# Kernel optimization log

Measured on AMD Instinct MI355X. Metric: run time of the kernel, lower is better.

Reference implementation:

```python
import jax, jax.numpy as jnp
import numpy as np
import math

HIDDEN = 4096
N_HEADS = 32
N_KV_HEADS = 8
HEAD_DIM = HIDDEN // N_HEADS  # 128
N_GROUPS = N_HEADS // N_KV_HEADS  # 4
ROPE_THETA = 10000.0


def setup_inputs() -> dict:
    key = jax.random.key(0)
    ks = jax.random.split(key, 5)
    B, S = 2, 2048
    hidden_states = jax.random.normal(ks[0], (B, S, HIDDEN), dtype=jnp.float32)
    position_ids = jnp.broadcast_to(jnp.arange(S, dtype=jnp.int32)[None, :], (B, S))
    sc = 1.0 / math.sqrt(HIDDEN)
    Wq = jax.random.normal(ks[1], (HIDDEN, N_HEADS * HEAD_DIM), dtype=jnp.float32) * sc
    Wk = jax.random.normal(ks[2], (HIDDEN, N_KV_HEADS * HEAD_DIM), dtype=jnp.float32) * sc
    Wv = jax.random.normal(ks[3], (HIDDEN, N_KV_HEADS * HEAD_DIM), dtype=jnp.float32) * sc
    Wo = jax.random.normal(ks[4], (HIDDEN, HIDDEN), dtype=jnp.float32) * sc
    return {"hidden_states": hidden_states, "position_ids": position_ids,
            "Wq": Wq, "Wk": Wk, "Wv": Wv, "Wo": Wo}


def _rope_cos_sin(position_ids):
    # inv_freq: [head_dim//2]
    inv_freq = 1.0 / (ROPE_THETA ** (jnp.arange(0, HEAD_DIM, 2, dtype=jnp.float32) / HEAD_DIM))
    freqs = position_ids.astype(jnp.float32)[..., None] * inv_freq  # [B, S, hd/2]
    emb = jnp.concatenate([freqs, freqs], axis=-1)  # [B, S, hd]
    return jnp.cos(emb), jnp.sin(emb)


def _rotate_half(x):
    h = x.shape[-1] // 2
    return jnp.concatenate([-x[..., h:], x[..., :h]], axis=-1)


def _apply_rope(x, cos, sin):
    # x: [B, H, S, hd]; cos/sin: [B, S, hd] -> unsqueeze head dim
    return x * cos[:, None] + _rotate_half(x) * sin[:, None]


def reference(hidden_states, position_ids, Wq, Wk, Wv, Wo):
    B, S, _ = hidden_states.shape
    q = (hidden_states @ Wq).reshape(B, S, N_HEADS, HEAD_DIM).transpose(0, 2, 1, 3)
    k = (hidden_states @ Wk).reshape(B, S, N_KV_HEADS, HEAD_DIM).transpose(0, 2, 1, 3)
    v = (hidden_states @ Wv).reshape(B, S, N_KV_HEADS, HEAD_DIM).transpose(0, 2, 1, 3)

    cos, sin = _rope_cos_sin(position_ids)
    q = _apply_rope(q, cos, sin)
    k = _apply_rope(k, cos, sin)

    # repeat_kv: (B, kvH, S, d) -> (B, H, S, d)
    k = jnp.repeat(k, N_GROUPS, axis=1)
    v = jnp.repeat(v, N_GROUPS, axis=1)

    scores = jnp.einsum('bhqd,bhkd->bhqk', q, k) / math.sqrt(HEAD_DIM)
    causal = jnp.tril(jnp.ones((S, S), dtype=bool))
    neg = jnp.finfo(jnp.float32).min
    scores = jnp.where(causal[None, None], scores, neg)
    attn = jax.nn.softmax(scores.astype(jnp.float32), axis=-1).astype(q.dtype)

    out = jnp.einsum('bhqk,bhkd->bhqd', attn, v)
    out = out.transpose(0, 2, 1, 3).reshape(B, S, HIDDEN)
    return out @ Wo
```

## Files before the change

kernel.cpp:

```cpp
#include <hip/hip_runtime.h>
#include <hip/hip_bf16.h>
#include <math.h>

#define HIDDEN 4096
#define NH 32
#define NKV 8
#define HD 128
#define S_LEN 2048
#define BATCH 2
#define MROWS (BATCH * S_LEN)
#define QKVW 6144

typedef __attribute__((ext_vector_type(8))) __bf16 bf16x8;
typedef __attribute__((ext_vector_type(4))) float f32x4;

__device__ __forceinline__ f32x4 mfma16(bf16x8 a, bf16x8 b, f32x4 c) {
  return __builtin_amdgcn_mfma_f32_16x16x32_bf16(a, b, c, 0, 0, 0);
}

__device__ __forceinline__ void gload16(const __bf16* g, const __bf16* l) {
  __builtin_amdgcn_global_load_lds(
      (const __attribute__((address_space(1))) void*)g,
      (__attribute__((address_space(3))) void*)l, 16, 0, 0);
}

#define SBAR()                              \
  do {                                      \
    asm volatile("" ::: "memory");          \
    __builtin_amdgcn_s_barrier();           \
    asm volatile("" ::: "memory");          \
  } while (0)

#define VMCNT8() asm volatile("s_waitcnt vmcnt(8)" ::: "memory")
#define VMCNT6() asm volatile("s_waitcnt vmcnt(6)" ::: "memory")

__global__ __launch_bounds__(256) void cvt_kernel(const float* __restrict__ in,
                                                  __bf16* __restrict__ out, int n) {
  int i = (blockIdx.x * 256 + threadIdx.x) * 8;
  if (i >= n) return;
  float4 a = *reinterpret_cast<const float4*>(in + i);
  float4 b = *reinterpret_cast<const float4*>(in + i + 4);
  bf16x8 t;
  t[0] = (__bf16)a.x; t[1] = (__bf16)a.y; t[2] = (__bf16)a.z; t[3] = (__bf16)a.w;
  t[4] = (__bf16)b.x; t[5] = (__bf16)b.y; t[6] = (__bf16)b.z; t[7] = (__bf16)b.w;
  *reinterpret_cast<bf16x8*>(out + i) = t;
}

__global__ __launch_bounds__(256) void tcvt3_kernel(const float* __restrict__ Wq,
                                                    const float* __restrict__ Wk,
                                                    const float* __restrict__ Wv,
                                                    __bf16* __restrict__ Wt) {
  __shared__ float t[32][33];
  int z = blockIdx.z;
  const float* in;
  __bf16* out;
  int C;
  if (z == 0)      { in = Wq; out = Wt;                         C = 4096; }
  else if (z == 1) { in = Wk; out = Wt + (size_t)4096 * 4096;   C = 1024; }
  else             { in = Wv; out = Wt + (size_t)5120 * 4096;   C = 1024; }
  if ((int)blockIdx.x * 32 >= C) return;
  int tx = threadIdx.x, ty = threadIdx.y;
  int r0 = blockIdx.y * 32, c0 = blockIdx.x * 32;
#pragma unroll
  for (int i = 0; i < 4; i++)
    t[ty + i * 8][tx] = in[(size_t)(r0 + ty + i * 8) * C + c0 + tx];
  __syncthreads();
#pragma unroll
  for (int i = 0; i < 4; i++)
    out[(size_t)(c0 + ty + i * 8) * 4096 + r0 + tx] = (__bf16)t[tx][ty + i * 8];
}

__global__ __launch_bounds__(256) void tcvt_f32(const float* __restrict__ in,
                                                __bf16* __restrict__ out,
                                                int R, int C) {
  __shared__ float t[32][33];
  int tx = threadIdx.x, ty = threadIdx.y;
  int r0 = blockIdx.y * 32, c0 = blockIdx.x * 32;
#pragma unroll
  for (int i = 0; i < 4; i++)
    t[ty + i * 8][tx] = in[(size_t)(r0 + ty + i * 8) * C + c0 + tx];
  __syncthreads();
#pragma unroll
  for (int i = 0; i < 4; i++)
    out[(size_t)(c0 + ty + i * 8) * R + r0 + tx] = (__bf16)t[tx][ty + i * 8];
}

__global__ __launch_bounds__(256) void tvt_kernel(const __bf16* __restrict__ qkv,
                                                  __bf16* __restrict__ vt) {
  __shared__ __bf16 t[32][33];
  int tx = threadIdx.x, ty = threadIdx.y;
  int z = blockIdx.z;
  int b = z >> 3, kvh = z & 7;
  int kv0 = blockIdx.y * 32, d0 = blockIdx.x * 32;
#pragma unroll
  for (int i = 0; i < 4; i++)
    t[ty + i * 8][tx] =
        qkv[(size_t)(b * S_LEN + kv0 + ty + i * 8) * QKVW + 5120 + kvh * HD + d0 + tx];
  __syncthreads();
  int cperm = kv0 + 2 * (tx & 15) + (tx >> 4);
#pragma unroll
  for (int i = 0; i < 4; i++)
    vt[((size_t)z * HD + d0 + ty + i * 8) * S_LEN + cperm] = t[tx][ty + i * 8];
}

template<typename CT>
__global__ __launch_bounds__(512, 2) void gemm256(const __bf16* __restrict__ A,
                                                  const __bf16* __restrict__ Bt,
                                                  CT* __restrict__ C,
                                                  int K, int ldc, int nbx) {
  __shared__ char lds[131072];
  const int tid = threadIdx.x;
  const int l = tid & 63, w = tid >> 6;
  const int lrow = l & 15, lg = l >> 4;
  const int sw = (lrow & 7) << 4;

  int nwg = gridDim.x;
  int swz = (blockIdx.x & 7) * (nwg >> 3) + (blockIdx.x >> 3);
  int bx = swz % nbx, by = swz / nbx;
  int m0 = by * 256, n0 = bx * 256;

  const int rA = w * 8 + (l >> 3);
  const int csw = ((l & 7) ^ (l >> 3)) * 8;
  const __bf16* As_[2][2];
  const __bf16* Bs_[2][2];
#pragma unroll
  for (int h = 0; h < 2; h++)
#pragma unroll
    for (int p = 0; p < 2; p++) {
      As_[h][p] = A + (size_t)(m0 + h * 128 + p * 64 + rA) * K + csw;
      Bs_[h][p] = Bt + (size_t)(n0 + h * 128 + p * 64 + rA) * K + csw;
    }

  auto stageA = [&](int par, int h, int kt) {
#pragma unroll
    for (int p = 0; p < 2; p++)
      gload16(As_[h][p] + kt * 64,
              (const __bf16*)(lds + par * 32768 + h * 16384 + p * 8192 + w * 1024));
  };
  auto stageB = [&](int par, int h, int kt) {
#pragma unroll
    for (int p = 0; p < 2; p++)
      gload16(Bs_[h][p] + kt * 64,
              (const __bf16*)(lds + 65536 + par * 32768 + h * 16384 + p * 8192 + w * 1024));
  };

  const int arbase = (w >> 2) * 64 + lrow;
  const int brbase = (w & 3) * 32 + lrow;

  bf16x8 aA[4][2];
  bf16x8 bB[2][2][2];

  auto readA = [&](int par, int ah) {
#pragma unroll
    for (int i = 0; i < 4; i++)
#pragma unroll
      for (int kk = 0; kk < 2; kk++)
        aA[i][kk] = *reinterpret_cast<const bf16x8*>(
            lds + par * 32768 + (arbase + i * 16 + ah * 128) * 128 +
            ((kk * 64 + lg * 16) ^ sw));
  };
  auto readB = [&](int par, int bh) {
#pragma unroll
    for (int j = 0; j < 2; j++)
#pragma unroll
      for (int kk = 0; kk < 2; kk++)
        bB[bh][j][kk] = *reinterpret_cast<const bf16x8*>(
            lds + 65536 + par * 32768 + (brbase + j * 16 + bh * 128) * 128 +
            ((kk * 64 + lg * 16) ^ sw));
  };

  f32x4 acc[8][4];
#pragma unroll
  for (int i = 0; i < 8; i++)
#pragma unroll
    for (int j = 0; j < 4; j++) {
      acc[i][j][0] = 0.f; acc[i][j][1] = 0.f; acc[i][j][2] = 0.f; acc[i][j][3] = 0.f;
    }

  const int NT = K >> 6;

  stageA(0, 0, 0); stageB(0, 0, 0);
  stageA(0, 1, 0); stageB(0, 1, 0);
  stageA(1, 0, 1); stageB(1, 0, 1);
  VMCNT8();
  SBAR();

#define MFMA_QUAD(AH, BH)                                                   \
  __builtin_amdgcn_s_setprio(1);                                            \
  _Pragma("unroll") for (int i4 = 0; i4 < 4; i4++)                          \
      _Pragma("unroll") for (int j2 = 0; j2 < 2; j2++)                      \
          _Pragma("unroll") for (int kk = 0; kk < 2; kk++)                  \
              acc[(AH)*4 + i4][(BH)*2 + j2] =                               \
                  mfma16(aA[i4][kk], bB[BH][j2][kk], acc[(AH)*4 + i4][(BH)*2 + j2]); \
  __builtin_amdgcn_s_setprio(0);

#define GTILE256(PAR, TT)                                                   \
  {                                                                         \
    const int t1n = ((TT) + 1 < NT) ? (TT) + 1 : 0;                         \
    const int t2n = ((TT) + 2 < NT) ? (TT) + 2 : 0;                         \
    readA(PAR, 0);                                                          \
    readB(PAR, 0);                                                          \
    stageA(PAR ^ 1, 1, t1n);                                                \
    stageB(PAR ^ 1, 1, t1n);                                                \
    VMCNT8();                                                               \
    SBAR();                                                                 \
    MFMA_QUAD(0, 0);                                                        \
    SBAR();                                                                 \
    readB(PAR, 1);                                                          \
    stageA(PAR, 0, t2n);                                                    \
    SBAR();                                                                 \
    MFMA_QUAD(0, 1);                                                        \
    SBAR();                                                                 \
    readA(PAR, 1);                                                          \
    stageB(PAR, 0, t2n);                                                    \
    SBAR();                                                                 \
    MFMA_QUAD(1, 0);                                                        \
    MFMA_QUAD(1, 1);                                                        \
    VMCNT8();                                                               \
    SBAR();                                                                 \
  }

  for (int t = 0; t < NT; t += 2) {
    GTILE256(0, t);
    GTILE256(1, t + 1);
  }
#undef GTILE256
#undef MFMA_QUAD

#pragma unroll
  for (int i = 0; i < 8; i++) {
    int row = m0 + (w >> 2) * 64 + (i & 3) * 16 + (i >> 2) * 128 + lg * 4;
#pragma unroll
    for (int j = 0; j < 4; j++) {
      int col = n0 + (w & 3) * 32 + (j & 1) * 16 + (j >> 1) * 128 + lrow;
#pragma unroll
      for (int jj = 0; jj < 4; jj++)
        C[(size_t)(row + jj) * ldc + col] = (CT)acc[i][j][jj];
    }
  }
}

template<typename CT>
__global__ __launch_bounds__(512, 2) void gemm128(const __bf16* __restrict__ A,
                                                  const __bf16* __restrict__ Bt,
                                                  CT* __restrict__ C,
                                                  int K, int ldc, int nbx) {
  __shared__ char lds[98304];
  const int tid = threadIdx.x;
  const int l = tid & 63, w = tid >> 6;
  const int lrow = l & 15, lg = l >> 4;
  const int sw = (lrow & 7) << 4;

  int nwg = gridDim.x;
  int swz = (blockIdx.x & 7) * (nwg >> 3) + (blockIdx.x >> 3);
  int bx = swz % nbx, by = swz / nbx;
  int m0 = by * 256, n0 = bx * 128;

  const int rA = w * 8 + (l >> 3);
  const int csw = ((l & 7) ^ (l >> 3)) * 8;
  const __bf16* As_[2][2];
  const __bf16* Bs_[2];
#pragma unroll
  for (int h = 0; h < 2; h++)
#pragma unroll
    for (int p = 0; p < 2; p++)
      As_[h][p] = A + (size_t)(m0 + h * 128 + p * 64 + rA) * K + csw;
#pragma unroll
  for (int p = 0; p < 2; p++)
    Bs_[p] = Bt + (size_t)(n0 + p * 64 + rA) * K + csw;

  auto stageA = [&](int par, int h, int kt) {
#pragma unroll
    for (int p = 0; p < 2; p++)
      gload16(As_[h][p] + kt * 64,
              (const __bf16*)(lds + par * 32768 + h * 16384 + p * 8192 + w * 1024));
  };
  auto stageB = [&](int par, int kt) {
#pragma unroll
    for (int p = 0; p < 2; p++)
      gload16(Bs_[p] + kt * 64,
              (const __bf16*)(lds + 65536 + par * 16384 + p * 8192 + w * 1024));
  };

  const int arbase = (w >> 2) * 64 + lrow;
  const int brbase = (w & 3) * 32 + lrow;

  bf16x8 aA[4][2];
  bf16x8 bB[2][2];

  auto readA = [&](int par, int ah) {
#pragma unroll
    for (int i = 0; i < 4; i++)
#pragma unroll
      for (int kk = 0; kk < 2; kk++)
        aA[i][kk] = *reinterpret_cast<const bf16x8*>(
            lds + par * 32768 + (arbase + i * 16 + ah * 128) * 128 +
            ((kk * 64 + lg * 16) ^ sw));
  };
  auto readB = [&](int par) {
#pragma unroll
    for (int j = 0; j < 2; j++)
#pragma unroll
      for (int kk = 0; kk < 2; kk++)
        bB[j][kk] = *reinterpret_cast<const bf16x8*>(
            lds + 65536 + par * 16384 + (brbase + j * 16) * 128 +
            ((kk * 64 + lg * 16) ^ sw));
  };

  f32x4 acc[8][2];
#pragma unroll
  for (int i = 0; i < 8; i++)
#pragma unroll
    for (int j = 0; j < 2; j++) {
      acc[i][j][0] = 0.f; acc[i][j][1] = 0.f; acc[i][j][2] = 0.f; acc[i][j][3] = 0.f;
    }

  const int NT = K >> 6;

  stageA(0, 0, 0); stageB(0, 0);
  stageA(0, 1, 0); stageB(1, 1); stageA(1, 0, 1);
  VMCNT6();
  SBAR();

#define MFMA_HALF(AH)                                                        \
  __builtin_amdgcn_s_setprio(1);                                             \
  _Pragma("unroll") for (int i4 = 0; i4 < 4; i4++)                           \
      _Pragma("unroll") for (int j2 = 0; j2 < 2; j2++)                       \
          _Pragma("unroll") for (int kk = 0; kk < 2; kk++)                   \
              acc[(AH)*4 + i4][j2] =                                         \
                  mfma16(aA[i4][kk], bB[j2][kk], acc[(AH)*4 + i4][j2]);      \
  __builtin_amdgcn_s_setprio(0);

#define GTILE128(PAR, TT)                                                    \
  {                                                                          \
    const int t1n = ((TT) + 1 < NT) ? (TT) + 1 : 0;                          \
    const int t2n = ((TT) + 2 < NT) ? (TT) + 2 : 0;                          \
    readA(PAR, 0);                                                           \
    readB(PAR);                                                              \
    stageA(PAR ^ 1, 1, t1n);                                                 \
    VMCNT6();                                                                \
    SBAR();                                                                  \
    MFMA_HALF(0);                                                            \
    SBAR();                                                                  \
    readA(PAR, 1);                                                           \
    stageB(PAR, t2n);                                                        \
    stageA(PAR, 0, t2n);                                                     \
    SBAR();                                                                  \
    MFMA_HALF(1);                                                            \
    VMCNT6();                                                                \
    SBAR();                                                                  \
  }

  for (int t = 0; t < NT; t += 2) {
    GTILE128(0, t);
    GTILE128(1, t + 1);
  }
#undef GTILE128
#undef MFMA_HALF

#pragma unroll
  for (int i = 0; i < 8; i++) {
    int row = m0 + (w >> 2) * 64 + (i & 3) * 16 + (i >> 2) * 128 + lg * 4;
#pragma unroll
    for (int j = 0; j < 2; j++) {
      int col = n0 + (w & 3) * 32 + j * 16 + lrow;
#pragma unroll
      for (int jj = 0; jj < 4; jj++)
        C[(size_t)(row + jj) * ldc + col] = (CT)acc[i][j][jj];
    }
  }
}

__global__ __launch_bounds__(256) void ropek_kernel(__bf16* __restrict__ qkv,
                                                    const int* __restrict__ pos) {
  int row = blockIdx.x * 4 + (threadIdx.x >> 6);
  int t = threadIdx.x & 63;
  float p = (float)pos[row];
  int head = t >> 3, chunk = t & 7;
  __bf16* base = qkv + (size_t)row * QKVW + 4096 + head * HD + chunk * 8;
  bf16x8 x1 = *reinterpret_cast<const bf16x8*>(base);
  bf16x8 x2 = *reinterpret_cast<const bf16x8*>(base + 64);
  bf16x8 o1, o2;
#pragma unroll
  for (int e = 0; e < 8; e++) {
    float ang = p * exp2f(-0.20762050f * (float)(chunk * 8 + e));
    float s, c;
    __sincosf(ang, &s, &c);
    float a = (float)x1[e], b2 = (float)x2[e];
    o1[e] = (__bf16)(a * c - b2 * s);
    o2[e] = (__bf16)(b2 * c + a * s);
  }
  *reinterpret_cast<bf16x8*>(base) = o1;
  *reinterpret_cast<bf16x8*>(base + 64) = o2;
}

__global__ __launch_bounds__(512) void attn_kernel(const __bf16* __restrict__ qkv,
                                                   const __bf16* __restrict__ vt,
                                                   const int* __restrict__ pos,
                                                   __bf16* __restrict__ out) {
  __shared__ __bf16 Ks[64 * 128];
  __shared__ __bf16 Vs[128 * 64];

  int tid = threadIdx.x;
  int l = tid & 63, w = tid >> 6;
  int bid = blockIdx.x;
  int qblk = 7 - (bid >> 6);
  int rem = bid & 63;
  int h = rem & 31, b = rem >> 5;
  int kvh = h >> 2;
  int q0w = qblk * 256 + w * 32;
  int lrow = l & 15, lg = l >> 4;
  int sw = (lrow & 7) << 4;
  const float SCL = 0.08838834764831845f * 1.4426950408889634f;

  const __bf16* kbase = qkv + (size_t)(b * S_LEN) * QKVW + 4096 + kvh * HD;
  const __bf16* vbase = vt + ((size_t)(b * NKV + kvh) * HD) * S_LEN;

  int krow = tid >> 3;
  int kslot = (tid & 7) * 2;
  int vrow = tid >> 2;
  int vslot = (tid & 3) * 2;
  char* KsB = (char*)Ks;
  char* VsB = (char*)Vs;
  int koff0 = krow * 256 + ((kslot * 16) ^ ((krow & 7) << 4));
  int koff1 = krow * 256 + (((kslot + 1) * 16) ^ ((krow & 7) << 4));
  int voff0 = vrow * 128 + ((vslot * 16) ^ ((vrow & 7) << 4));
  int voff1 = vrow * 128 + (((vslot + 1) * 16) ^ ((vrow & 7) << 4));
  const __bf16* kg = kbase + (size_t)krow * QKVW + kslot * 8;
  const __bf16* vg = vbase + (size_t)vrow * S_LEN + vslot * 8;

  bf16x8 qf[2][4];
#pragma unroll
  for (int mi = 0; mi < 2; mi++) {
    int qrow = q0w + mi * 16 + lrow;
    const __bf16* qp = qkv + (size_t)(b * S_LEN + qrow) * QKVW + h * HD + lg * 8;
    float p = (float)pos[b * S_LEN + qrow];
#pragma unroll
    for (int kk = 0; kk < 2; kk++) {
      bf16x8 xlo = *reinterpret_cast<const bf16x8*>(qp + kk * 32);
      bf16x8 xhi = *reinterpret_cast<const bf16x8*>(qp + (kk + 2) * 32);
      bf16x8 olo, ohi;
#pragma unroll
      for (int e = 0; e < 8; e++) {
        int d = kk * 32 + lg * 8 + e;
        float ang = p * exp2f(-0.20762050f * (float)d);
        float s, c;
        __sincosf(ang, &s, &c);
        c *= SCL; s *= SCL;
        float a = (float)xlo[e], b2 = (float)xhi[e];
        olo[e] = (__bf16)(a * c - b2 * s);
        ohi[e] = (__bf16)(b2 * c + a * s);
      }
      qf[mi][kk] = olo;
      qf[mi][kk + 2] = ohi;
    }
  }

  f32x4 ov[2][8];
#pragma unroll
  for (int mi = 0; mi < 2; mi++)
#pragma unroll
    for (int n = 0; n < 8; n++) {
      ov[mi][n][0] = 0.f; ov[mi][n][1] = 0.f; ov[mi][n][2] = 0.f; ov[mi][n][3] = 0.f;
    }
  float m[2], ssum[2];
  m[0] = -3.0e38f; m[1] = -3.0e38f;
  ssum[0] = 0.f; ssum[1] = 0.f;

  int nt = 4 * qblk + 4;
  bf16x8 kr0, kr1, vr0, vr1;

  kr0 = *reinterpret_cast<const bf16x8*>(kg);
  kr1 = *reinterpret_cast<const bf16x8*>(kg + 8);
  vr0 = *reinterpret_cast<const bf16x8*>(vg);
  vr1 = *reinterpret_cast<const bf16x8*>(vg + 8);
  *reinterpret_cast<bf16x8*>(KsB + koff0) = kr0;
  *reinterpret_cast<bf16x8*>(KsB + koff1) = kr1;
  *reinterpret_cast<bf16x8*>(VsB + voff0) = vr0;
  *reinterpret_cast<bf16x8*>(VsB + voff1) = vr1;
  __syncthreads();

  for (int t = 0;; t++) {
    int kv0 = t * 64;
    bool more = (t + 1 < nt);
    if (more) {
      int kvn = kv0 + 64;
      kr0 = *reinterpret_cast<const bf16x8*>(kg + (size_t)kvn * QKVW);
      kr1 = *reinterpret_cast<const bf16x8*>(kg + (size_t)kvn * QKVW + 8);
      vr0 = *reinterpret_cast<const bf16x8*>(vg + kvn);
      vr1 = *reinterpret_cast<const bf16x8*>(vg + kvn + 8);
    }

    bool active = (kv0 <= q0w + 31);
    if (active) {
      f32x4 sc[2][4];
#pragma unroll
      for (int mi = 0; mi < 2; mi++)
#pragma unroll
        for (int c = 0; c < 4; c++) {
          sc[mi][c][0] = 0.f; sc[mi][c][1] = 0.f; sc[mi][c][2] = 0.f; sc[mi][c][3] = 0.f;
        }
#pragma unroll
      for (int c = 0; c < 4; c++) {
        int rb = (c * 16 + lrow) * 256;
#pragma unroll
        for (int kk = 0; kk < 4; kk++) {
          bf16x8 kf = *reinterpret_cast<const bf16x8*>(KsB + rb + ((kk * 64 + lg * 16) ^ sw));
          sc[0][c] = mfma16(kf, qf[0][kk], sc[0][c]);
          sc[1][c] = mfma16(kf, qf[1][kk], sc[1][c]);
        }
      }

      bool bound = (kv0 + 64 > q0w);
      if (bound) {
#pragma unroll
        for (int mi = 0; mi < 2; mi++) {
          int qidx = q0w + mi * 16 + lrow;
#pragma unroll
          for (int jj = 0; jj < 4; jj++) {
            int kvb = kv0 + lg * 4 + jj;
            if (kvb > qidx)      sc[mi][0][jj] = -3.0e38f;
            if (kvb + 16 > qidx) sc[mi][1][jj] = -3.0e38f;
            if (kvb + 32 > qidx) sc[mi][2][jj] = -3.0e38f;
            if (kvb + 48 > qidx) sc[mi][3][jj] = -3.0e38f;
          }
        }
      }

      float lm[2];
      bool lanegrow = false;
#pragma unroll
      for (int mi = 0; mi < 2; mi++) {
        float a0 = fmaxf(fmaxf(sc[mi][0][0], sc[mi][0][1]), fmaxf(sc[mi][0][2], sc[mi][0][3]));
        float a1 = fmaxf(fmaxf(sc[mi][1][0], sc[mi][1][1]), fmaxf(sc[mi][1][2], sc[mi][1][3]));
        float a2 = fmaxf(fmaxf(sc[mi][2][0], sc[mi][2][1]), fmaxf(sc[mi][2][2], sc[mi][2][3]));
        float a3 = fmaxf(fmaxf(sc[mi][3][0], sc[mi][3][1]), fmaxf(sc[mi][3][2], sc[mi][3][3]));
        lm[mi] = fmaxf(fmaxf(a0, a1), fmaxf(a2, a3));
        lanegrow |= (lm[mi] > m[mi] + 8.0f);
      }

      if (__any(lanegrow)) {
        float es[2];
#pragma unroll
        for (int mi = 0; mi < 2; mi++) {
          float r = lm[mi];
          r = fmaxf(r, __shfl_xor(r, 16));
          r = fmaxf(r, __shfl_xor(r, 32));
          float mo = m[mi];
          bool grow = (r > mo + 8.0f);
          float mn = grow ? r : mo;
          float e = grow ? exp2f(mo - r) : 1.0f;
          es[mi] = e;
          m[mi] = mn;
          ssum[mi] *= e;
        }
        float esv[2][4];
#pragma unroll
        for (int mi = 0; mi < 2; mi++)
#pragma unroll
          for (int jj = 0; jj < 4; jj++)
            esv[mi][jj] = __shfl(es[mi], lg * 4 + jj);
#pragma unroll
        for (int mi = 0; mi < 2; mi++)
#pragma unroll
          for (int n = 0; n < 8; n++)
#pragma unroll
            for (int jj = 0; jj < 4; jj++) ov[mi][n][jj] *= esv[mi][jj];
      }

      bf16x8 pa[2][2];
#pragma unroll
      for (int mi = 0; mi < 2; mi++) {
        float mn = m[mi];
#pragma unroll
        for (int c = 0; c < 4; c++)
#pragma unroll
          for (int r = 0; r < 4; r++) {
            float p = exp2f(sc[mi][c][r] - mn);
            ssum[mi] += p;
            pa[mi][c >> 1][(r << 1) | (c & 1)] = (__bf16)p;
          }
      }

#pragma unroll
      for (int kvs = 0; kvs < 2; kvs++) {
#pragma unroll
        for (int n = 0; n < 8; n++) {
          bf16x8 vf = *reinterpret_cast<const bf16x8*>(
              VsB + (n * 16 + lrow) * 128 + ((kvs * 64 + lg * 16) ^ sw));
          ov[0][n] = mfma16(pa[0][kvs], vf, ov[0][n]);
          ov[1][n] = mfma16(pa[1][kvs], vf, ov[1][n]);
        }
      }
    }

    if (!more) break;
    __syncthreads();
    *reinterpret_cast<bf16x8*>(KsB + koff0) = kr0;
    *reinterpret_cast<bf16x8*>(KsB + koff1) = kr1;
    *reinterpret_cast<bf16x8*>(VsB + voff0) = vr0;
    *reinterpret_cast<bf16x8*>(VsB + voff1) = vr1;
    __syncthreads();
  }

  float rs[2];
#pragma unroll
  for (int mi = 0; mi < 2; mi++) {
    float s = ssum[mi];
    s += __shfl_xor(s, 16);
    s += __shfl_xor(s, 32);
    rs[mi] = s;
  }
  float rinv[2][4];
#pragma unroll
  for (int mi = 0; mi < 2; mi++)
#pragma unroll
    for (int jj = 0; jj < 4; jj++)
      rinv[mi][jj] = 1.0f / __shfl(rs[mi], lg * 4 + jj);
#pragma unroll
  for (int mi = 0; mi < 2; mi++)
#pragma unroll
    for (int n = 0; n < 8; n++)
#pragma unroll
      for (int jj = 0; jj < 4; jj++) {
        out[(size_t)(b * S_LEN + q0w + mi * 16 + lg * 4 + jj) * HIDDEN + h * HD + n * 16 + lrow] =
            (__bf16)(ov[mi][n][jj] * rinv[mi][jj]);
      }
}

extern "C" void kernel_launch(void* const* d_in, const int* in_sizes, int n_in,
                              void* d_out, int out_size, void* d_ws, size_t ws_size,
                              hipStream_t stream) {
  const float* hidden = (const float*)d_in[0];
  const int* posids   = (const int*)d_in[1];
  const float* Wq     = (const float*)d_in[2];
  const float* Wk     = (const float*)d_in[3];
  const float* Wv     = (const float*)d_in[4];
  const float* Wo     = (const float*)d_in[5];
  float* out = (float*)d_out;

  char* ws = (char*)d_ws;
  __bf16* h_bf    = (__bf16*)(ws + 0);
  __bf16* a_buf   = h_bf;
  __bf16* Wt      = (__bf16*)(ws + 33554432);
  __bf16* qkv_buf = (__bf16*)(ws + 83886080);
  __bf16* vt_buf  = (__bf16*)(ws + 134217728);

  dim3 b256(256), b328(32, 8), b512(512);

  cvt_kernel<<<dim3(MROWS * HIDDEN / (256 * 8)), b256, 0, stream>>>(hidden, h_bf, MROWS * HIDDEN);

  tcvt3_kernel<<<dim3(128, 128, 3), b328, 0, stream>>>(Wq, Wk, Wv, Wt);

  gemm256<__bf16><<<dim3(256), b512, 0, stream>>>(
      h_bf, Wt, qkv_buf, HIDDEN, QKVW, 4096 / 256);
  gemm128<__bf16><<<dim3(256), b512, 0, stream>>>(
      h_bf, Wt + (size_t)4096 * 4096, qkv_buf + 4096, HIDDEN, QKVW, 2048 / 128);

  ropek_kernel<<<dim3(MROWS / 4), b256, 0, stream>>>(qkv_buf, posids);

  tvt_kernel<<<dim3(HD / 32, S_LEN / 32, BATCH * NKV), b328, 0, stream>>>(qkv_buf, vt_buf);

  attn_kernel<<<dim3(8 * NH * BATCH), b512, 0, stream>>>(qkv_buf, vt_buf, posids, a_buf);

  tcvt_f32<<<dim3(HIDDEN / 32, HIDDEN / 32), b328, 0, stream>>>(Wo, Wt, HIDDEN, HIDDEN);

  gemm256<float><<<dim3(256), b512, 0, stream>>>(
      a_buf, Wt, out, HIDDEN, HIDDEN, HIDDEN / 256);
}
```

Baseline: 451.2 us.

## Double-buffer attention K/V tiles in LDS via direct global-to-LDS loads

Replaces the register-staged K/V prefetch (global load to registers, then LDS store between two barriers) with global_load_lds directly into a double-buffered 64KB LDS region. The swizzle moves to the global address side so the LDS layout matches the existing read pattern. Each iteration now needs one vmcnt(0) wait and one barrier instead of two barriers plus LDS stores, and registers are freed. The cost is twice the LDS footprint, which may limit blocks per CU.

```diff
diff --git a/kernel.cpp b/kernel.cpp
--- a/kernel.cpp
+++ b/kernel.cpp
@@ -33,6 +33,7 @@
 
 #define VMCNT8() asm volatile("s_waitcnt vmcnt(8)" ::: "memory")
 #define VMCNT6() asm volatile("s_waitcnt vmcnt(6)" ::: "memory")
+#define VMCNT0() asm volatile("s_waitcnt vmcnt(0)" ::: "memory")
 
 __global__ __launch_bounds__(256) void cvt_kernel(const float* __restrict__ in,
                                                   __bf16* __restrict__ out, int n) {
@@ -398,8 +399,7 @@
                                                    const __bf16* __restrict__ vt,
                                                    const int* __restrict__ pos,
                                                    __bf16* __restrict__ out) {
-  __shared__ __bf16 Ks[64 * 128];
-  __shared__ __bf16 Vs[128 * 64];
+  __shared__ char lds[65536];
 
   int tid = threadIdx.x;
   int l = tid & 63, w = tid >> 6;
@@ -416,18 +416,24 @@
   const __bf16* kbase = qkv + (size_t)(b * S_LEN) * QKVW + 4096 + kvh * HD;
   const __bf16* vbase = vt + ((size_t)(b * NKV + kvh) * HD) * S_LEN;
 
-  int krow = tid >> 3;
-  int kslot = (tid & 7) * 2;
-  int vrow = tid >> 2;
-  int vslot = (tid & 3) * 2;
-  char* KsB = (char*)Ks;
-  char* VsB = (char*)Vs;
-  int koff0 = krow * 256 + ((kslot * 16) ^ ((krow & 7) << 4));
-  int koff1 = krow * 256 + (((kslot + 1) * 16) ^ ((krow & 7) << 4));
-  int voff0 = vrow * 128 + ((vslot * 16) ^ ((vrow & 7) << 4));
-  int voff1 = vrow * 128 + (((vslot + 1) * 16) ^ ((vrow & 7) << 4));
-  const __bf16* kg = kbase + (size_t)krow * QKVW + kslot * 8;
-  const __bf16* vg = vbase + (size_t)vrow * S_LEN + vslot * 8;
+  int rK0 = 8 * w + (l >> 4), rK1 = rK0 + 4;
+  int cK0 = (l & 8) | (((l & 7) ^ (rK0 & 7)) & 7);
+  int cK1 = (l & 8) | (((l & 7) ^ (rK1 & 7)) & 7);
+  const __bf16* kgs0 = kbase + (size_t)rK0 * QKVW + cK0 * 8;
+  const __bf16* kgs1 = kbase + (size_t)rK1 * QKVW + cK1 * 8;
+  int rV0 = 16 * w + (l >> 3), rV1 = rV0 + 8;
+  int cV0 = (l & 7) ^ (rV0 & 7);
+  int cV1 = (l & 7) ^ (rV1 & 7);
+  const __bf16* vgs0 = vbase + (size_t)rV0 * S_LEN + cV0 * 8;
+  const __bf16* vgs1 = vbase + (size_t)rV1 * S_LEN + cV1 * 8;
+
+  auto stageKV = [&](int par, int kvn) {
+    size_t ko = (size_t)kvn * QKVW;
+    gload16(kgs0 + ko, (const __bf16*)(lds + par * 16384 + w * 2048));
+    gload16(kgs1 + ko, (const __bf16*)(lds + par * 16384 + w * 2048 + 1024));
+    gload16(vgs0 + kvn, (const __bf16*)(lds + 32768 + par * 16384 + w * 2048));
+    gload16(vgs1 + kvn, (const __bf16*)(lds + 32768 + par * 16384 + w * 2048 + 1024));
+  };
 
   bf16x8 qf[2][4];
 #pragma unroll
@@ -468,28 +474,16 @@
   ssum[0] = 0.f; ssum[1] = 0.f;
 
   int nt = 4 * qblk + 4;
-  bf16x8 kr0, kr1, vr0, vr1;
-
-  kr0 = *reinterpret_cast<const bf16x8*>(kg);
-  kr1 = *reinterpret_cast<const bf16x8*>(kg + 8);
-  vr0 = *reinterpret_cast<const bf16x8*>(vg);
-  vr1 = *reinterpret_cast<const bf16x8*>(vg + 8);
-  *reinterpret_cast<bf16x8*>(KsB + koff0) = kr0;
-  *reinterpret_cast<bf16x8*>(KsB + koff1) = kr1;
-  *reinterpret_cast<bf16x8*>(VsB + voff0) = vr0;
-  *reinterpret_cast<bf16x8*>(VsB + voff1) = vr1;
+
+  stageKV(0, 0);
+  VMCNT0();
   __syncthreads();
 
   for (int t = 0;; t++) {
     int kv0 = t * 64;
     bool more = (t + 1 < nt);
-    if (more) {
-      int kvn = kv0 + 64;
-      kr0 = *reinterpret_cast<const bf16x8*>(kg + (size_t)kvn * QKVW);
-      kr1 = *reinterpret_cast<const bf16x8*>(kg + (size_t)kvn * QKVW + 8);
-      vr0 = *reinterpret_cast<const bf16x8*>(vg + kvn);
-      vr1 = *reinterpret_cast<const bf16x8*>(vg + kvn + 8);
-    }
+    if (more) stageKV((t + 1) & 1, kv0 + 64);
+    int pb = (t & 1) * 16384;
 
     bool active = (kv0 <= q0w + 31);
     if (active) {
@@ -502,10 +496,10 @@
         }
 #pragma unroll
       for (int c = 0; c < 4; c++) {
-        int rb = (c * 16 + lrow) * 256;
+        int rb = pb + (c * 16 + lrow) * 256;
 #pragma unroll
         for (int kk = 0; kk < 4; kk++) {
-          bf16x8 kf = *reinterpret_cast<const bf16x8*>(KsB + rb + ((kk * 64 + lg * 16) ^ sw));
+          bf16x8 kf = *reinterpret_cast<const bf16x8*>(lds + rb + ((kk * 64 + lg * 16) ^ sw));
           sc[0][c] = mfma16(kf, qf[0][kk], sc[0][c]);
           sc[1][c] = mfma16(kf, qf[1][kk], sc[1][c]);
         }
@@ -587,7 +581,7 @@
 #pragma unroll
         for (int n = 0; n < 8; n++) {
           bf16x8 vf = *reinterpret_cast<const bf16x8*>(
-              VsB + (n * 16 + lrow) * 128 + ((kvs * 64 + lg * 16) ^ sw));
+              lds + 32768 + pb + (n * 16 + lrow) * 128 + ((kvs * 64 + lg * 16) ^ sw));
           ov[0][n] = mfma16(pa[0][kvs], vf, ov[0][n]);
           ov[1][n] = mfma16(pa[1][kvs], vf, ov[1][n]);
         }
@@ -595,11 +589,7 @@
     }
 
     if (!more) break;
-    __syncthreads();
-    *reinterpret_cast<bf16x8*>(KsB + koff0) = kr0;
-    *reinterpret_cast<bf16x8*>(KsB + koff1) = kr1;
-    *reinterpret_cast<bf16x8*>(VsB + voff0) = vr0;
-    *reinterpret_cast<bf16x8*>(VsB + voff1) = vr1;
+    VMCNT0();
     __syncthreads();
   }
 
```

After: 452.5 us. Within noise of the previous version (+0.3%).

## Halve attention query tile to 128 rows per block, 16 per wave

Applied to the files above, without the earlier changes.

The attention kernel now gives each block 128 query rows instead of 256, with each wave handling one 16-row MFMA tile instead of two. The grid doubles to 1024 blocks, which should improve load balance across CUs for the causal triangle and lower per-thread register use. In exchange, each K/V tile loaded into LDS is reused by half as many query rows, so K/V traffic doubles and there is less MFMA work per LDS read.

```diff
diff --git a/kernel.cpp b/kernel.cpp
--- a/kernel.cpp
+++ b/kernel.cpp
@@ -404,11 +404,11 @@
   int tid = threadIdx.x;
   int l = tid & 63, w = tid >> 6;
   int bid = blockIdx.x;
-  int qblk = 7 - (bid >> 6);
+  int qblk = 15 - (bid >> 6);
   int rem = bid & 63;
   int h = rem & 31, b = rem >> 5;
   int kvh = h >> 2;
-  int q0w = qblk * 256 + w * 32;
+  int q0w = qblk * 128 + w * 16;
   int lrow = l & 15, lg = l >> 4;
   int sw = (lrow & 7) << 4;
   const float SCL = 0.08838834764831845f * 1.4426950408889634f;
@@ -429,10 +429,9 @@
   const __bf16* kg = kbase + (size_t)krow * QKVW + kslot * 8;
   const __bf16* vg = vbase + (size_t)vrow * S_LEN + vslot * 8;
 
-  bf16x8 qf[2][4];
-#pragma unroll
-  for (int mi = 0; mi < 2; mi++) {
-    int qrow = q0w + mi * 16 + lrow;
+  bf16x8 qf[4];
+  {
+    int qrow = q0w + lrow;
     const __bf16* qp = qkv + (size_t)(b * S_LEN + qrow) * QKVW + h * HD + lg * 8;
     float p = (float)pos[b * S_LEN + qrow];
 #pragma unroll
@@ -451,23 +450,19 @@
         olo[e] = (__bf16)(a * c - b2 * s);
         ohi[e] = (__bf16)(b2 * c + a * s);
       }
-      qf[mi][kk] = olo;
-      qf[mi][kk + 2] = ohi;
-    }
-  }
-
-  f32x4 ov[2][8];
-#pragma unroll
-  for (int mi = 0; mi < 2; mi++)
-#pragma unroll
-    for (int n = 0; n < 8; n++) {
-      ov[mi][n][0] = 0.f; ov[mi][n][1] = 0.f; ov[mi][n][2] = 0.f; ov[mi][n][3] = 0.f;
-    }
-  float m[2], ssum[2];
-  m[0] = -3.0e38f; m[1] = -3.0e38f;
-  ssum[0] = 0.f; ssum[1] = 0.f;
-
-  int nt = 4 * qblk + 4;
+      qf[kk] = olo;
+      qf[kk + 2] = ohi;
+    }
+  }
+
+  f32x4 ov[8];
+#pragma unroll
+  for (int n = 0; n < 8; n++) {
+    ov[n][0] = 0.f; ov[n][1] = 0.f; ov[n][2] = 0.f; ov[n][3] = 0.f;
+  }
+  float m = -3.0e38f, ssum = 0.f;
+
+  int nt = 2 * qblk + 2;
   bf16x8 kr0, kr1, vr0, vr1;
 
   kr0 = *reinterpret_cast<const bf16x8*>(kg);
@@ -491,96 +486,72 @@
       vr1 = *reinterpret_cast<const bf16x8*>(vg + kvn + 8);
     }
 
-    bool active = (kv0 <= q0w + 31);
+    bool active = (kv0 <= q0w + 15);
     if (active) {
-      f32x4 sc[2][4];
-#pragma unroll
-      for (int mi = 0; mi < 2; mi++)
-#pragma unroll
-        for (int c = 0; c < 4; c++) {
-          sc[mi][c][0] = 0.f; sc[mi][c][1] = 0.f; sc[mi][c][2] = 0.f; sc[mi][c][3] = 0.f;
-        }
+      f32x4 sc[4];
+#pragma unroll
+      for (int c = 0; c < 4; c++) {
+        sc[c][0] = 0.f; sc[c][1] = 0.f; sc[c][2] = 0.f; sc[c][3] = 0.f;
+      }
 #pragma unroll
       for (int c = 0; c < 4; c++) {
         int rb = (c * 16 + lrow) * 256;
 #pragma unroll
         for (int kk = 0; kk < 4; kk++) {
           bf16x8 kf = *reinterpret_cast<const bf16x8*>(KsB + rb + ((kk * 64 + lg * 16) ^ sw));
-          sc[0][c] = mfma16(kf, qf[0][kk], sc[0][c]);
-          sc[1][c] = mfma16(kf, qf[1][kk], sc[1][c]);
+          sc[c] = mfma16(kf, qf[kk], sc[c]);
         }
       }
 
       bool bound = (kv0 + 64 > q0w);
       if (bound) {
-#pragma unroll
-        for (int mi = 0; mi < 2; mi++) {
-          int qidx = q0w + mi * 16 + lrow;
-#pragma unroll
-          for (int jj = 0; jj < 4; jj++) {
-            int kvb = kv0 + lg * 4 + jj;
-            if (kvb > qidx)      sc[mi][0][jj] = -3.0e38f;
-            if (kvb + 16 > qidx) sc[mi][1][jj] = -3.0e38f;
-            if (kvb + 32 > qidx) sc[mi][2][jj] = -3.0e38f;
-            if (kvb + 48 > qidx) sc[mi][3][jj] = -3.0e38f;
-          }
+        int qidx = q0w + lrow;
+#pragma unroll
+        for (int jj = 0; jj < 4; jj++) {
+          int kvb = kv0 + lg * 4 + jj;
+          if (kvb > qidx)      sc[0][jj] = -3.0e38f;
+          if (kvb + 16 > qidx) sc[1][jj] = -3.0e38f;
+          if (kvb + 32 > qidx) sc[2][jj] = -3.0e38f;
+          if (kvb + 48 > qidx) sc[3][jj] = -3.0e38f;
         }
       }
 
-      float lm[2];
-      bool lanegrow = false;
-#pragma unroll
-      for (int mi = 0; mi < 2; mi++) {
-        float a0 = fmaxf(fmaxf(sc[mi][0][0], sc[mi][0][1]), fmaxf(sc[mi][0][2], sc[mi][0][3]));
-        float a1 = fmaxf(fmaxf(sc[mi][1][0], sc[mi][1][1]), fmaxf(sc[mi][1][2], sc[mi][1][3]));
-        float a2 = fmaxf(fmaxf(sc[mi][2][0], sc[mi][2][1]), fmaxf(sc[mi][2][2], sc[mi][2][3]));
-        float a3 = fmaxf(fmaxf(sc[mi][3][0], sc[mi][3][1]), fmaxf(sc[mi][3][2], sc[mi][3][3]));
-        lm[mi] = fmaxf(fmaxf(a0, a1), fmaxf(a2, a3));
-        lanegrow |= (lm[mi] > m[mi] + 8.0f);
+      float a0 = fmaxf(fmaxf(sc[0][0], sc[0][1]), fmaxf(sc[0][2], sc[0][3]));
+      float a1 = fmaxf(fmaxf(sc[1][0], sc[1][1]), fmaxf(sc[1][2], sc[1][3]));
+      float a2 = fmaxf(fmaxf(sc[2][0], sc[2][1]), fmaxf(sc[2][2], sc[2][3]));
+      float a3 = fmaxf(fmaxf(sc[3][0], sc[3][1]), fmaxf(sc[3][2], sc[3][3]));
+      float lm = fmaxf(fmaxf(a0, a1), fmaxf(a2, a3));
+      bool lanegrow = (lm > m + 8.0f);
+
+      if (__any(lanegrow)) {
+        float r = lm;
+        r = fmaxf(r, __shfl_xor(r, 16));
+        r = fmaxf(r, __shfl_xor(r, 32));
+        float mo = m;
+        bool grow = (r > mo + 8.0f);
+        float mn = grow ? r : mo;
+        float e = grow ? exp2f(mo - r) : 1.0f;
+        m = mn;
+        ssum *= e;
+        float esv[4];
+#pragma unroll
+        for (int jj = 0; jj < 4; jj++)
+          esv[jj] = __shfl(e, lg * 4 + jj);
+#pragma unroll
+        for (int n = 0; n < 8; n++)
+#pragma unroll
+          for (int jj = 0; jj < 4; jj++) ov[n][jj] *= esv[jj];
       }
 
-      if (__any(lanegrow)) {
-        float es[2];
-#pragma unroll
-        for (int mi = 0; mi < 2; mi++) {
-          float r = lm[mi];
-          r = fmaxf(r, __shfl_xor(r, 16));
-          r = fmaxf(r, __shfl_xor(r, 32));
-          float mo = m[mi];
-          bool grow = (r > mo + 8.0f);
-          float mn = grow ? r : mo;
-          float e = grow ? exp2f(mo - r) : 1.0f;
-          es[mi] = e;
-          m[mi] = mn;
-          ssum[mi] *= e;
+      bf16x8 pa[2];
+#pragma unroll
+      for (int c = 0; c < 4; c++)
+#pragma unroll
+        for (int r = 0; r < 4; r++) {
+          float p = exp2f(sc[c][r] - m);
+          ssum += p;
+          pa[c >> 1][(r << 1) | (c & 1)] = (__bf16)p;
         }
-        float esv[2][4];
-#pragma unroll
-        for (int mi = 0; mi < 2; mi++)
-#pragma unroll
-          for (int jj = 0; jj < 4; jj++)
-            esv[mi][jj] = __shfl(es[mi], lg * 4 + jj);
-#pragma unroll
-        for (int mi = 0; mi < 2; mi++)
-#pragma unroll
-          for (int n = 0; n < 8; n++)
-#pragma unroll
-            for (int jj = 0; jj < 4; jj++) ov[mi][n][jj] *= esv[mi][jj];
-      }
-
-      bf16x8 pa[2][2];
-#pragma unroll
-      for (int mi = 0; mi < 2; mi++) {
-        float mn = m[mi];
-#pragma unroll
-        for (int c = 0; c < 4; c++)
-#pragma unroll
-          for (int r = 0; r < 4; r++) {
-            float p = exp2f(sc[mi][c][r] - mn);
-            ssum[mi] += p;
-            pa[mi][c >> 1][(r << 1) | (c & 1)] = (__bf16)p;
-          }
-      }
 
 #pragma unroll
       for (int kvs = 0; kvs < 2; kvs++) {
@@ -588,8 +559,7 @@
         for (int n = 0; n < 8; n++) {
           bf16x8 vf = *reinterpret_cast<const bf16x8*>(
               VsB + (n * 16 + lrow) * 128 + ((kvs * 64 + lg * 16) ^ sw));
-          ov[0][n] = mfma16(pa[0][kvs], vf, ov[0][n]);
-          ov[1][n] = mfma16(pa[1][kvs], vf, ov[1][n]);
+          ov[n] = mfma16(pa[kvs], vf, ov[n]);
         }
       }
     }
@@ -603,29 +573,20 @@
     __syncthreads();
   }
 
-  float rs[2];
-#pragma unroll
-  for (int mi = 0; mi < 2; mi++) {
-    float s = ssum[mi];
-    s += __shfl_xor(s, 16);
-    s += __shfl_xor(s, 32);
-    rs[mi] = s;
-  }
-  float rinv[2][4];
-#pragma unroll
-  for (int mi = 0; mi < 2; mi++)
-#pragma unroll
-    for (int jj = 0; jj < 4; jj++)
-      rinv[mi][jj] = 1.0f / __shfl(rs[mi], lg * 4 + jj);
-#pragma unroll
-  for (int mi = 0; mi < 2; mi++)
-#pragma unroll
-    for (int n = 0; n < 8; n++)
-#pragma unroll
-      for (int jj = 0; jj < 4; jj++) {
-        out[(size_t)(b * S_LEN + q0w + mi * 16 + lg * 4 + jj) * HIDDEN + h * HD + n * 16 + lrow] =
-            (__bf16)(ov[mi][n][jj] * rinv[mi][jj]);
-      }
+  float s = ssum;
+  s += __shfl_xor(s, 16);
+  s += __shfl_xor(s, 32);
+  float rinv[4];
+#pragma unroll
+  for (int jj = 0; jj < 4; jj++)
+    rinv[jj] = 1.0f / __shfl(s, lg * 4 + jj);
+#pragma unroll
+  for (int n = 0; n < 8; n++)
+#pragma unroll
+    for (int jj = 0; jj < 4; jj++) {
+      out[(size_t)(b * S_LEN + q0w + lg * 4 + jj) * HIDDEN + h * HD + n * 16 + lrow] =
+          (__bf16)(ov[n][jj] * rinv[jj]);
+    }
 }
 
 extern "C" void kernel_launch(void* const* d_in, const int* in_sizes, int n_in,
@@ -661,7 +622,7 @@
 
   tvt_kernel<<<dim3(HD / 32, S_LEN / 32, BATCH * NKV), b328, 0, stream>>>(qkv_buf, vt_buf);
 
-  attn_kernel<<<dim3(8 * NH * BATCH), b512, 0, stream>>>(qkv_buf, vt_buf, posids, a_buf);
+  attn_kernel<<<dim3(16 * NH * BATCH), b512, 0, stream>>>(qkv_buf, vt_buf, posids, a_buf);
 
   tcvt_f32<<<dim3(HIDDEN / 32, HIDDEN / 32), b328, 0, stream>>>(Wo, Wt, HIDDEN, HIDDEN);
 
```

After: 453.9 us. About the same (+0.6%).
